# Kernel optimization log

Hardware: AMD Instinct MI355X
Metric: run time of the kernel (lower is better)

Reference implementation:

```python
import jax, jax.numpy as jnp
import numpy as np

N, H, M, B = 64, 64, 32, 16384
relu = jax.nn.relu


def setup_inputs() -> dict:
    key = jax.random.key(0)
    ks = jax.random.split(key, 10)
    s = 0.05
    x = jax.random.normal(ks[0], (B, N), dtype=jnp.float32)
    # stacked per-node weights (torch Linear applies x @ W.T, W: [out, in])
    W1a = jax.random.normal(ks[1], (N, H, N), dtype=jnp.float32) * s   # directed net layer 1
    W1b = jax.random.normal(ks[2], (N, M, H), dtype=jnp.float32) * s   # directed net layer 2
    W2a = jax.random.normal(ks[3], (N, H, N), dtype=jnp.float32) * s   # bi-directed net layer 1
    W2b = jax.random.normal(ks[4], (N, M, H), dtype=jnp.float32) * s   # bi-directed net layer 2
    W3a = jax.random.normal(ks[5], (N, H, 2 * M + N), dtype=jnp.float32) * s  # fuse layer 1
    b3a = jax.random.normal(ks[6], (N, H), dtype=jnp.float32) * s
    W3b = jax.random.normal(ks[7], (N, 1, H), dtype=jnp.float32) * s          # fuse layer 2
    b3b = jax.random.normal(ks[8], (N, 1), dtype=jnp.float32) * s
    return {"x": x, "W1a": W1a, "W1b": W1b, "W2a": W2a, "W2b": W2b,
            "W3a": W3a, "b3a": b3a, "W3b": W3b, "b3b": b3b}


def reference(x, W1a, W1b, W2a, W2b, W3a, b3a, W3b, b3b):
    Bsz, n = x.shape
    eye = jnp.eye(n, dtype=x.dtype)
    off = 1.0 - eye  # filter_1; adjacency at init is also (ones - eye), so mask is idempotent
    # inputs_1_dag / inputs_1_bi: [B, N, N] per-node masked copies of x
    x1 = jnp.einsum('bn,in->bin', x, off)
    # inputs_2: [B, N, N] with x[b,i] on the diagonal of row i
    x2 = eye[None, :, :] * x[:, None, :]
    # directed branch: ReLU(Linear) -> ReLU(Linear), batched over node i
    r1 = relu(jnp.einsum('bih,imh->bim', relu(jnp.einsum('bin,ihn->bih', x1, W1a)), W1b))
    # bi-directed branch (same masked input at init)
    r2 = relu(jnp.einsum('bih,imh->bim', relu(jnp.einsum('bin,ihn->bih', x1, W2a)), W2b))
    feat = jnp.concatenate([r1, r2, x2], axis=2)  # [B, N, 2M+N]
    h = relu(jnp.einsum('bik,ihk->bih', feat, W3a) + b3a[None])
    out = relu(jnp.einsum('bih,ioh->bio', h, W3b) + b3b[None])  # [B, N, 1]
    return out[..., 0]  # [B, N] causal derivative
```

## Files before the change

kernel.cpp:

```cpp
#include <hip/hip_runtime.h>


typedef short bf16x8 __attribute__((ext_vector_type(8)));
typedef float f32x4  __attribute__((ext_vector_type(4)));
typedef unsigned int u32x4 __attribute__((ext_vector_type(4)));

__device__ __forceinline__ unsigned int pack2(float a, float b) {
    union { float f; unsigned int u; } ua, ub; ua.f = a; ub.f = b;
    return __builtin_amdgcn_perm(ub.u + 0x8000u, ua.u + 0x8000u, 0x07060302u);
}

__device__ __forceinline__ f32x4 mfma16(bf16x8 a, bf16x8 b, f32x4 c) {
    return __builtin_amdgcn_mfma_f32_16x16x32_bf16(a, b, c, 0, 0, 0);
}

__device__ __forceinline__ bf16x8 pack_frag(f32x4 lo, f32x4 hi) {
    union { u32x4 u; bf16x8 v; } r;
    r.u[0] = pack2(fmaxf(lo[0], 0.f), fmaxf(lo[1], 0.f));
    r.u[1] = pack2(fmaxf(lo[2], 0.f), fmaxf(lo[3], 0.f));
    r.u[2] = pack2(fmaxf(hi[0], 0.f), fmaxf(hi[1], 0.f));
    r.u[3] = pack2(fmaxf(hi[2], 0.f), fmaxf(hi[3], 0.f));
    return r.v;
}

__device__ __forceinline__ bf16x8 cvt_frag2(const float* __restrict__ plo,
                                            const float* __restrict__ phi) {
    f32x4 f0 = *(const f32x4*)plo;
    f32x4 f1 = *(const f32x4*)phi;
    union { u32x4 u; bf16x8 v; } r;
    r.u[0] = pack2(f0[0], f0[1]);
    r.u[1] = pack2(f0[2], f0[3]);
    r.u[2] = pack2(f1[0], f1[1]);
    r.u[3] = pack2(f1[2], f1[3]);
    return r.v;
}

__device__ __forceinline__ bf16x8 cvt_frag2_m(const float* __restrict__ plo,
                                              const float* __restrict__ phi,
                                              const unsigned int* M) {
    f32x4 f0 = *(const f32x4*)plo;
    f32x4 f1 = *(const f32x4*)phi;
    union { u32x4 u; bf16x8 v; } r;
    r.u[0] = pack2(f0[0], f0[1]) & M[0];
    r.u[1] = pack2(f0[2], f0[3]) & M[1];
    r.u[2] = pack2(f1[0], f1[1]) & M[2];
    r.u[3] = pack2(f1[2], f1[3]) & M[3];
    return r.v;
}

__global__ __launch_bounds__(256) void prep_x(const float* __restrict__ x,
                                              unsigned short* __restrict__ xb) {
    int j = (blockIdx.x * 256 + threadIdx.x) * 8;
    f32x4 a = *(const f32x4*)&x[j];
    f32x4 b = *(const f32x4*)&x[j + 4];
    u32x4 r = { pack2(a[0], a[1]), pack2(a[2], a[3]), pack2(b[0], b[1]), pack2(b[2], b[3]) };
    *(u32x4*)&xb[j] = r;
}

__global__ __launch_bounds__(256, 2) void main_kernel(
    const float* __restrict__ x,
    const float* __restrict__ W1a, const float* __restrict__ W1b,
    const float* __restrict__ W2a, const float* __restrict__ W2b,
    const float* __restrict__ W3a, const float* __restrict__ b3a,
    const float* __restrict__ W3b, const float* __restrict__ b3b,
    const unsigned short* __restrict__ xb,
    float* __restrict__ out)
{
    const int i    = blockIdx.x & 63;
    const int bg   = blockIdx.x >> 6;
    const int tid  = threadIdx.x;
    const int w    = tid >> 6;
    const int lane = tid & 63;
    const int q    = lane >> 4;
    const int c0   = lane & 15;

    unsigned int M[2][4];
    {
        const unsigned int halfmask = (i & 1) ? 0x0000FFFFu : 0xFFFF0000u;
        const int dz = (i >> 1) & 3;
        #pragma unroll
        for (int s = 0; s < 2; ++s) {
            bool hit = ((i >> 3) == s * 4 + q);
            #pragma unroll
            for (int d = 0; d < 4; ++d)
                M[s][d] = (hit && d == dz) ? halfmask : 0xFFFFFFFFu;
        }
    }

    bf16x8 A1[4][2], A2[4][2];
    {
        const float* p1 = W1a + (i << 12);
        const float* p2 = W2a + (i << 12);
        #pragma unroll
        for (int t = 0; t < 4; ++t)
            #pragma unroll
            for (int s = 0; s < 2; ++s) {
                int off = (((t << 4) + c0) << 6) + (s << 5) + (q << 3);
                A1[t][s] = cvt_frag2_m(p1 + off, p1 + off + 4, M[s]);
                A2[t][s] = cvt_frag2_m(p2 + off, p2 + off + 4, M[s]);
            }
    }
    bf16x8 F1[2][2], F2[2][2];
    {
        const float* p1 = W1b + (i << 11);
        const float* p2 = W2b + (i << 11);
        #pragma unroll
        for (int t = 0; t < 2; ++t)
            #pragma unroll
            for (int s = 0; s < 2; ++s) {
                int base = (((t << 4) + c0) << 6) + (s << 5) + (q << 2);
                F1[t][s] = cvt_frag2(p1 + base, p1 + base + 16);
                F2[t][s] = cvt_frag2(p2 + base, p2 + base + 16);
            }
    }
    bf16x8 A3[4][2];
    {
        const float* p3 = W3a + (i << 13);
        #pragma unroll
        for (int t = 0; t < 4; ++t)
            #pragma unroll
            for (int s = 0; s < 2; ++s) {
                int base = (((t << 4) + c0) << 7) + (s << 5) + (q << 2);
                A3[t][s] = cvt_frag2(p3 + base, p3 + base + 16);
            }
    }
    f32x4 b3av[4], w3xv[4], w3bv[4];
    #pragma unroll
    for (int t = 0; t < 4; ++t) {
        int h0 = (i << 6) + (t << 4) + (q << 2);
        b3av[t] = *(const f32x4*)&b3a[h0];
        w3bv[t] = *(const f32x4*)&W3b[h0];
        #pragma unroll
        for (int r = 0; r < 4; ++r)
            w3xv[t][r] = W3a[(i << 13) + (((t << 4) + (q << 2) + r) << 7) + 64 + i];
    }
    const float bb = b3b[i];

    const int rbase0 = (((bg << 2) + w) << 9);

    int row = rbase0 + c0;
    bf16x8 XB0 = *(const bf16x8*)&xb[(row << 6) + (q << 3)];
    bf16x8 XB1 = *(const bf16x8*)&xb[(row << 6) + 32 + (q << 3)];
    float   xd = x[(row << 6) + i];

    for (int k = 0; k < 32; ++k) {
        int nrow = rbase0 + ((k < 31 ? k + 1 : 31) << 4) + c0;
        bf16x8 nXB0 = *(const bf16x8*)&xb[(nrow << 6) + (q << 3)];
        bf16x8 nXB1 = *(const bf16x8*)&xb[(nrow << 6) + 32 + (q << 3)];
        float   nxd = x[(nrow << 6) + i];

        f32x4 a1[4], a2[4];
        #pragma unroll
        for (int t = 0; t < 4; ++t) {
            f32x4 z = {0.f, 0.f, 0.f, 0.f};
            f32x4 u = mfma16(A1[t][0], XB0, z);
            a1[t]   = mfma16(A1[t][1], XB1, u);
            f32x4 v = mfma16(A2[t][0], XB0, z);
            a2[t]   = mfma16(A2[t][1], XB1, v);
        }
        bf16x8 HB0 = pack_frag(a1[0], a1[1]);
        bf16x8 HB1 = pack_frag(a1[2], a1[3]);
        bf16x8 GB0 = pack_frag(a2[0], a2[1]);
        bf16x8 GB1 = pack_frag(a2[2], a2[3]);

        f32x4 b1[2], b2[2];
        #pragma unroll
        for (int t = 0; t < 2; ++t) {
            f32x4 z = {0.f, 0.f, 0.f, 0.f};
            f32x4 u = mfma16(F1[t][0], HB0, z);
            b1[t]   = mfma16(F1[t][1], HB1, u);
            f32x4 v = mfma16(F2[t][0], GB0, z);
            b2[t]   = mfma16(F2[t][1], GB1, v);
        }
        bf16x8 RB0 = pack_frag(b1[0], b1[1]);
        bf16x8 RB1 = pack_frag(b2[0], b2[1]);

        float p = 0.f;
        #pragma unroll
        for (int t = 0; t < 4; ++t) {
            f32x4 acc;
            #pragma unroll
            for (int r = 0; r < 4; ++r) acc[r] = fmaf(xd, w3xv[t][r], b3av[t][r]);
            acc = mfma16(A3[t][0], RB0, acc);
            acc = mfma16(A3[t][1], RB1, acc);
            #pragma unroll
            for (int r = 0; r < 4; ++r) p = fmaf(fmaxf(acc[r], 0.f), w3bv[t][r], p);
        }
        p += __shfl_xor(p, 16);
        p += __shfl_xor(p, 32);
        if (lane < 16) out[(row << 6) + i] = fmaxf(p + bb, 0.f);

        row = nrow; XB0 = nXB0; XB1 = nXB1; xd = nxd;
    }
}

extern "C" void kernel_launch(void* const* d_in, const int* in_sizes, int n_in,
                              void* d_out, int out_size, void* d_ws, size_t ws_size,
                              hipStream_t stream) {
    (void)in_sizes; (void)n_in; (void)out_size; (void)ws_size;
    const float* x   = (const float*)d_in[0];
    const float* W1a = (const float*)d_in[1];
    const float* W1b = (const float*)d_in[2];
    const float* W2a = (const float*)d_in[3];
    const float* W2b = (const float*)d_in[4];
    const float* W3a = (const float*)d_in[5];
    const float* b3a = (const float*)d_in[6];
    const float* W3b = (const float*)d_in[7];
    const float* b3b = (const float*)d_in[8];
    float* out = (float*)d_out;
    unsigned short* xb = (unsigned short*)d_ws;

    prep_x<<<512, 256, 0, stream>>>(x, xb);
    main_kernel<<<512, 256, 0, stream>>>(x, W1a, W1b, W2a, W2b, W3a, b3a, W3b, b3b, xb, out);
}
```

Before: 131.7 us.

## Specialize waves into a three-stage LDS pipeline and fuse x conversion

Splits the per-block work so two waves compute the first layers of each branch, one wave computes the second layers, and one wave computes the fuse layer. Intermediate activations pass through double-buffered shared memory with a block barrier each step. This cuts the per-wave weight register footprint and removes the separate bf16 conversion kernel for x, which is now converted in-register. In exchange it adds a barrier per step, pipeline fill and drain steps, and stores the fuse x-weights in bf16.

New measurement: 171.6 us. 1.3x slower.

```diff
diff --git a/kernel.cpp b/kernel.cpp
--- a/kernel.cpp
+++ b/kernel.cpp
@@ -5,9 +5,18 @@
 typedef float f32x4  __attribute__((ext_vector_type(4)));
 typedef unsigned int u32x4 __attribute__((ext_vector_type(4)));
 
+#define CHUNKS 64
+
 __device__ __forceinline__ unsigned int pack2(float a, float b) {
     union { float f; unsigned int u; } ua, ub; ua.f = a; ub.f = b;
     return __builtin_amdgcn_perm(ub.u + 0x8000u, ua.u + 0x8000u, 0x07060302u);
+}
+
+__device__ __forceinline__ float bf_lo(unsigned int u) {
+    union { unsigned int u; float f; } v; v.u = u << 16; return v.f;
+}
+__device__ __forceinline__ float bf_hi(unsigned int u) {
+    union { unsigned int u; float f; } v; v.u = u & 0xFFFF0000u; return v.f;
 }
 
 __device__ __forceinline__ f32x4 mfma16(bf16x8 a, bf16x8 b, f32x4 c) {
@@ -23,16 +32,18 @@
     return r.v;
 }
 
+__device__ __forceinline__ bf16x8 pack_vals(f32x4 lo, f32x4 hi) {
+    union { u32x4 u; bf16x8 v; } r;
+    r.u[0] = pack2(lo[0], lo[1]);
+    r.u[1] = pack2(lo[2], lo[3]);
+    r.u[2] = pack2(hi[0], hi[1]);
+    r.u[3] = pack2(hi[2], hi[3]);
+    return r.v;
+}
+
 __device__ __forceinline__ bf16x8 cvt_frag2(const float* __restrict__ plo,
                                             const float* __restrict__ phi) {
-    f32x4 f0 = *(const f32x4*)plo;
-    f32x4 f1 = *(const f32x4*)phi;
-    union { u32x4 u; bf16x8 v; } r;
-    r.u[0] = pack2(f0[0], f0[1]);
-    r.u[1] = pack2(f0[2], f0[3]);
-    r.u[2] = pack2(f1[0], f1[1]);
-    r.u[3] = pack2(f1[2], f1[3]);
-    return r.v;
+    return pack_vals(*(const f32x4*)plo, *(const f32x4*)phi);
 }
 
 __device__ __forceinline__ bf16x8 cvt_frag2_m(const float* __restrict__ plo,
@@ -48,31 +59,23 @@
     return r.v;
 }
 
-__global__ __launch_bounds__(256) void prep_x(const float* __restrict__ x,
-                                              unsigned short* __restrict__ xb) {
-    int j = (blockIdx.x * 256 + threadIdx.x) * 8;
-    f32x4 a = *(const f32x4*)&x[j];
-    f32x4 b = *(const f32x4*)&x[j + 4];
-    u32x4 r = { pack2(a[0], a[1]), pack2(a[2], a[3]), pack2(b[0], b[1]), pack2(b[2], b[3]) };
-    *(u32x4*)&xb[j] = r;
-}
-
 __global__ __launch_bounds__(256, 2) void main_kernel(
     const float* __restrict__ x,
     const float* __restrict__ W1a, const float* __restrict__ W1b,
     const float* __restrict__ W2a, const float* __restrict__ W2b,
     const float* __restrict__ W3a, const float* __restrict__ b3a,
     const float* __restrict__ W3b, const float* __restrict__ b3b,
-    const unsigned short* __restrict__ xb,
     float* __restrict__ out)
 {
+    __shared__ unsigned short lds[6144];
+
     const int i    = blockIdx.x & 63;
     const int bg   = blockIdx.x >> 6;
-    const int tid  = threadIdx.x;
-    const int w    = tid >> 6;
-    const int lane = tid & 63;
+    const int w    = threadIdx.x >> 6;
+    const int lane = threadIdx.x & 63;
     const int q    = lane >> 4;
     const int c0   = lane & 15;
+    const int rowbase = bg << 10;
 
     unsigned int M[2][4];
     {
@@ -87,21 +90,17 @@
         }
     }
 
-    bf16x8 A1[4][2], A2[4][2];
-    {
-        const float* p1 = W1a + (i << 12);
-        const float* p2 = W2a + (i << 12);
+    bf16x8 W[8];
+    if (w < 2) {
+        const float* p = (w == 0 ? W1a : W2a) + (i << 12);
         #pragma unroll
         for (int t = 0; t < 4; ++t)
             #pragma unroll
             for (int s = 0; s < 2; ++s) {
                 int off = (((t << 4) + c0) << 6) + (s << 5) + (q << 3);
-                A1[t][s] = cvt_frag2_m(p1 + off, p1 + off + 4, M[s]);
-                A2[t][s] = cvt_frag2_m(p2 + off, p2 + off + 4, M[s]);
-            }
-    }
-    bf16x8 F1[2][2], F2[2][2];
-    {
+                W[t * 2 + s] = cvt_frag2_m(p + off, p + off + 4, M[s]);
+            }
+    } else if (w == 2) {
         const float* p1 = W1b + (i << 11);
         const float* p2 = W2b + (i << 11);
         #pragma unroll
@@ -109,95 +108,128 @@
             #pragma unroll
             for (int s = 0; s < 2; ++s) {
                 int base = (((t << 4) + c0) << 6) + (s << 5) + (q << 2);
-                F1[t][s] = cvt_frag2(p1 + base, p1 + base + 16);
-                F2[t][s] = cvt_frag2(p2 + base, p2 + base + 16);
-            }
-    }
-    bf16x8 A3[4][2];
-    {
+                W[t * 2 + s]     = cvt_frag2(p1 + base, p1 + base + 16);
+                W[4 + t * 2 + s] = cvt_frag2(p2 + base, p2 + base + 16);
+            }
+    } else {
         const float* p3 = W3a + (i << 13);
         #pragma unroll
         for (int t = 0; t < 4; ++t)
             #pragma unroll
             for (int s = 0; s < 2; ++s) {
                 int base = (((t << 4) + c0) << 7) + (s << 5) + (q << 2);
-                A3[t][s] = cvt_frag2(p3 + base, p3 + base + 16);
-            }
-    }
-    f32x4 b3av[4], w3xv[4], w3bv[4];
-    #pragma unroll
-    for (int t = 0; t < 4; ++t) {
-        int h0 = (i << 6) + (t << 4) + (q << 2);
-        b3av[t] = *(const f32x4*)&b3a[h0];
-        w3bv[t] = *(const f32x4*)&W3b[h0];
-        #pragma unroll
-        for (int r = 0; r < 4; ++r)
-            w3xv[t][r] = W3a[(i << 13) + (((t << 4) + (q << 2) + r) << 7) + 64 + i];
-    }
-    const float bb = b3b[i];
-
-    const int rbase0 = (((bg << 2) + w) << 9);
-
-    int row = rbase0 + c0;
-    bf16x8 XB0 = *(const bf16x8*)&xb[(row << 6) + (q << 3)];
-    bf16x8 XB1 = *(const bf16x8*)&xb[(row << 6) + 32 + (q << 3)];
-    float   xd = x[(row << 6) + i];
-
-    for (int k = 0; k < 32; ++k) {
-        int nrow = rbase0 + ((k < 31 ? k + 1 : 31) << 4) + c0;
-        bf16x8 nXB0 = *(const bf16x8*)&xb[(nrow << 6) + (q << 3)];
-        bf16x8 nXB1 = *(const bf16x8*)&xb[(nrow << 6) + 32 + (q << 3)];
-        float   nxd = x[(nrow << 6) + i];
-
-        f32x4 a1[4], a2[4];
+                W[t * 2 + s] = cvt_frag2(p3 + base, p3 + base + 16);
+            }
+    }
+
+    f32x4 b3av[4], w3bv[4];
+    uint2 wxp[4];
+    float bb = 0.f, xd_n = 0.f;
+    if (w == 3) {
         #pragma unroll
         for (int t = 0; t < 4; ++t) {
-            f32x4 z = {0.f, 0.f, 0.f, 0.f};
-            f32x4 u = mfma16(A1[t][0], XB0, z);
-            a1[t]   = mfma16(A1[t][1], XB1, u);
-            f32x4 v = mfma16(A2[t][0], XB0, z);
-            a2[t]   = mfma16(A2[t][1], XB1, v);
+            int h0 = (i << 6) + (t << 4) + (q << 2);
+            b3av[t] = *(const f32x4*)&b3a[h0];
+            w3bv[t] = *(const f32x4*)&W3b[h0];
+            float v0 = W3a[(i << 13) + (((t << 4) + (q << 2) + 0) << 7) + 64 + i];
+            float v1 = W3a[(i << 13) + (((t << 4) + (q << 2) + 1) << 7) + 64 + i];
+            float v2 = W3a[(i << 13) + (((t << 4) + (q << 2) + 2) << 7) + 64 + i];
+            float v3 = W3a[(i << 13) + (((t << 4) + (q << 2) + 3) << 7) + 64 + i];
+            wxp[t].x = pack2(v0, v1);
+            wxp[t].y = pack2(v2, v3);
         }
-        bf16x8 HB0 = pack_frag(a1[0], a1[1]);
-        bf16x8 HB1 = pack_frag(a1[2], a1[3]);
-        bf16x8 GB0 = pack_frag(a2[0], a2[1]);
-        bf16x8 GB1 = pack_frag(a2[2], a2[3]);
-
-        f32x4 b1[2], b2[2];
-        #pragma unroll
-        for (int t = 0; t < 2; ++t) {
-            f32x4 z = {0.f, 0.f, 0.f, 0.f};
-            f32x4 u = mfma16(F1[t][0], HB0, z);
-            b1[t]   = mfma16(F1[t][1], HB1, u);
-            f32x4 v = mfma16(F2[t][0], GB0, z);
-            b2[t]   = mfma16(F2[t][1], GB1, v);
+        bb = b3b[i];
+        xd_n = x[((rowbase + c0) << 6) + i];
+    }
+
+    f32x4 xr0, xr1, xr2, xr3;
+    if (w < 2) {
+        const float* xp = x + ((rowbase + c0) << 6) + (q << 3);
+        xr0 = *(const f32x4*)xp;       xr1 = *(const f32x4*)(xp + 4);
+        xr2 = *(const f32x4*)(xp + 32); xr3 = *(const f32x4*)(xp + 36);
+    }
+
+    for (int k = 0; k < CHUNKS + 2; ++k) {
+        if (w < 2) {
+            if (k < CHUNKS) {
+                bf16x8 XB0 = pack_vals(xr0, xr1);
+                bf16x8 XB1 = pack_vals(xr2, xr3);
+                if (k + 1 < CHUNKS) {
+                    const float* xp = x + ((rowbase + ((k + 1) << 4) + c0) << 6) + (q << 3);
+                    xr0 = *(const f32x4*)xp;        xr1 = *(const f32x4*)(xp + 4);
+                    xr2 = *(const f32x4*)(xp + 32); xr3 = *(const f32x4*)(xp + 36);
+                }
+                f32x4 a[4];
+                #pragma unroll
+                for (int t = 0; t < 4; ++t) {
+                    f32x4 z = {0.f, 0.f, 0.f, 0.f};
+                    f32x4 u = mfma16(W[2 * t], XB0, z);
+                    a[t] = mfma16(W[2 * t + 1], XB1, u);
+                }
+                bf16x8 H0 = pack_frag(a[0], a[1]);
+                bf16x8 H1 = pack_frag(a[2], a[3]);
+                unsigned short* dst = &lds[(w << 11) + ((k & 1) << 10) + (lane << 3)];
+                *(bf16x8*)dst         = H0;
+                *(bf16x8*)(dst + 512) = H1;
+            }
+        } else if (w == 2) {
+            int k2 = k - 1;
+            if (k2 >= 0 && k2 < CHUNKS) {
+                const unsigned short* s1 = &lds[((k2 & 1) << 10) + (lane << 3)];
+                const unsigned short* s2 = s1 + 2048;
+                bf16x8 HB0 = *(const bf16x8*)s1, HB1 = *(const bf16x8*)(s1 + 512);
+                bf16x8 GB0 = *(const bf16x8*)s2, GB1 = *(const bf16x8*)(s2 + 512);
+                f32x4 b1[2], b2[2];
+                #pragma unroll
+                for (int t = 0; t < 2; ++t) {
+                    f32x4 z = {0.f, 0.f, 0.f, 0.f};
+                    f32x4 u = mfma16(W[2 * t], HB0, z);
+                    b1[t] = mfma16(W[2 * t + 1], HB1, u);
+                    f32x4 v = mfma16(W[4 + 2 * t], GB0, z);
+                    b2[t] = mfma16(W[5 + 2 * t], GB1, v);
+                }
+                bf16x8 R0 = pack_frag(b1[0], b1[1]);
+                bf16x8 R1 = pack_frag(b2[0], b2[1]);
+                unsigned short* dst = &lds[4096 + ((k2 & 1) << 10) + (lane << 3)];
+                *(bf16x8*)dst         = R0;
+                *(bf16x8*)(dst + 512) = R1;
+            }
+        } else {
+            int k3 = k - 2;
+            if (k3 >= 0) {
+                float xdc = xd_n;
+                if (k3 + 1 < CHUNKS)
+                    xd_n = x[((rowbase + ((k3 + 1) << 4) + c0) << 6) + i];
+                const unsigned short* s = &lds[4096 + ((k3 & 1) << 10) + (lane << 3)];
+                bf16x8 RB0 = *(const bf16x8*)s, RB1 = *(const bf16x8*)(s + 512);
+                float p = 0.f;
+                #pragma unroll
+                for (int t = 0; t < 4; ++t) {
+                    f32x4 acc;
+                    acc[0] = fmaf(xdc, bf_lo(wxp[t].x), b3av[t][0]);
+                    acc[1] = fmaf(xdc, bf_hi(wxp[t].x), b3av[t][1]);
+                    acc[2] = fmaf(xdc, bf_lo(wxp[t].y), b3av[t][2]);
+                    acc[3] = fmaf(xdc, bf_hi(wxp[t].y), b3av[t][3]);
+                    acc = mfma16(W[2 * t], RB0, acc);
+                    acc = mfma16(W[2 * t + 1], RB1, acc);
+                    #pragma unroll
+                    for (int r = 0; r < 4; ++r)
+                        p = fmaf(fmaxf(acc[r], 0.f), w3bv[t][r], p);
+                }
+                p += __shfl_xor(p, 16);
+                p += __shfl_xor(p, 32);
+                if (lane < 16)
+                    out[((rowbase + (k3 << 4) + c0) << 6) + i] = fmaxf(p + bb, 0.f);
+            }
         }
-        bf16x8 RB0 = pack_frag(b1[0], b1[1]);
-        bf16x8 RB1 = pack_frag(b2[0], b2[1]);
-
-        float p = 0.f;
-        #pragma unroll
-        for (int t = 0; t < 4; ++t) {
-            f32x4 acc;
-            #pragma unroll
-            for (int r = 0; r < 4; ++r) acc[r] = fmaf(xd, w3xv[t][r], b3av[t][r]);
-            acc = mfma16(A3[t][0], RB0, acc);
-            acc = mfma16(A3[t][1], RB1, acc);
-            #pragma unroll
-            for (int r = 0; r < 4; ++r) p = fmaf(fmaxf(acc[r], 0.f), w3bv[t][r], p);
-        }
-        p += __shfl_xor(p, 16);
-        p += __shfl_xor(p, 32);
-        if (lane < 16) out[(row << 6) + i] = fmaxf(p + bb, 0.f);
-
-        row = nrow; XB0 = nXB0; XB1 = nXB1; xd = nxd;
+        __syncthreads();
     }
 }
 
 extern "C" void kernel_launch(void* const* d_in, const int* in_sizes, int n_in,
                               void* d_out, int out_size, void* d_ws, size_t ws_size,
                               hipStream_t stream) {
-    (void)in_sizes; (void)n_in; (void)out_size; (void)ws_size;
+    (void)in_sizes; (void)n_in; (void)out_size; (void)d_ws; (void)ws_size;
     const float* x   = (const float*)d_in[0];
     const float* W1a = (const float*)d_in[1];
     const float* W1b = (const float*)d_in[2];
@@ -208,8 +240,6 @@
     const float* W3b = (const float*)d_in[7];
     const float* b3b = (const float*)d_in[8];
     float* out = (float*)d_out;
-    unsigned short* xb = (unsigned short*)d_ws;
-
-    prep_x<<<512, 256, 0, stream>>>(x, xb);
-    main_kernel<<<512, 256, 0, stream>>>(x, W1a, W1b, W2a, W2b, W3a, b3a, W3b, b3b, xb, out);
-}
+
+    main_kernel<<<1024, 256, 0, stream>>>(x, W1a, W1b, W2a, W2b, W3a, b3a, W3b, b3b, out);
+}
```

## Replace final layer reduction with MFMA and interleave two row streams

Applied to the files above, without the earlier changes.

The final fuse-layer dot product with W3b, previously a per-lane FMA loop followed by two cross-lane shuffles, now runs as two MFMAs against a bf16 fragment of W3b. The W3a diagonal column is packed into bf16 pairs to save registers. The explicit software prefetch of the next row is removed and replaced by two independent row-tile computations per iteration, so the scheduler can overlap loads and MFMA chains. This lowers the final-layer precision to bf16 and relies on the compiler to hide load latency.

Result: slower. 138.0 us (+4.8%).

```diff
diff --git a/kernel.cpp b/kernel.cpp
--- a/kernel.cpp
+++ b/kernel.cpp
@@ -8,6 +8,13 @@
 __device__ __forceinline__ unsigned int pack2(float a, float b) {
     union { float f; unsigned int u; } ua, ub; ua.f = a; ub.f = b;
     return __builtin_amdgcn_perm(ub.u + 0x8000u, ua.u + 0x8000u, 0x07060302u);
+}
+
+__device__ __forceinline__ float bf_lo(unsigned int u) {
+    union { unsigned int u; float f; } v; v.u = u << 16; return v.f;
+}
+__device__ __forceinline__ float bf_hi(unsigned int u) {
+    union { unsigned int u; float f; } v; v.u = u & 0xFFFF0000u; return v.f;
 }
 
 __device__ __forceinline__ f32x4 mfma16(bf16x8 a, bf16x8 b, f32x4 c) {
@@ -124,39 +131,44 @@
                 A3[t][s] = cvt_frag2(p3 + base, p3 + base + 16);
             }
     }
-    f32x4 b3av[4], w3xv[4], w3bv[4];
+    bf16x8 WB[2];
+    {
+        const float* pb = W3b + (i << 6);
+        #pragma unroll
+        for (int s = 0; s < 2; ++s) {
+            int base = (s << 5) + (q << 2);
+            WB[s] = cvt_frag2(pb + base, pb + base + 16);
+        }
+    }
+    f32x4 b3av[4];
+    uint2  wxp[4];
     #pragma unroll
     for (int t = 0; t < 4; ++t) {
         int h0 = (i << 6) + (t << 4) + (q << 2);
         b3av[t] = *(const f32x4*)&b3a[h0];
-        w3bv[t] = *(const f32x4*)&W3b[h0];
-        #pragma unroll
-        for (int r = 0; r < 4; ++r)
-            w3xv[t][r] = W3a[(i << 13) + (((t << 4) + (q << 2) + r) << 7) + 64 + i];
+        float v0 = W3a[(i << 13) + (((t << 4) + (q << 2) + 0) << 7) + 64 + i];
+        float v1 = W3a[(i << 13) + (((t << 4) + (q << 2) + 1) << 7) + 64 + i];
+        float v2 = W3a[(i << 13) + (((t << 4) + (q << 2) + 2) << 7) + 64 + i];
+        float v3 = W3a[(i << 13) + (((t << 4) + (q << 2) + 3) << 7) + 64 + i];
+        wxp[t].x = pack2(v0, v1);
+        wxp[t].y = pack2(v2, v3);
     }
     const float bb = b3b[i];
 
-    const int rbase0 = (((bg << 2) + w) << 9);
-
-    int row = rbase0 + c0;
-    bf16x8 XB0 = *(const bf16x8*)&xb[(row << 6) + (q << 3)];
-    bf16x8 XB1 = *(const bf16x8*)&xb[(row << 6) + 32 + (q << 3)];
-    float   xd = x[(row << 6) + i];
-
-    for (int k = 0; k < 32; ++k) {
-        int nrow = rbase0 + ((k < 31 ? k + 1 : 31) << 4) + c0;
-        bf16x8 nXB0 = *(const bf16x8*)&xb[(nrow << 6) + (q << 3)];
-        bf16x8 nXB1 = *(const bf16x8*)&xb[(nrow << 6) + 32 + (q << 3)];
-        float   nxd = x[(nrow << 6) + i];
+    auto process = [&](int row) {
+        const unsigned short* xp = xb + (row << 6);
+        bf16x8 X0 = *(const bf16x8*)&xp[(q << 3)];
+        bf16x8 X1 = *(const bf16x8*)&xp[32 + (q << 3)];
+        float  xd = x[(row << 6) + i];
 
         f32x4 a1[4], a2[4];
         #pragma unroll
         for (int t = 0; t < 4; ++t) {
             f32x4 z = {0.f, 0.f, 0.f, 0.f};
-            f32x4 u = mfma16(A1[t][0], XB0, z);
-            a1[t]   = mfma16(A1[t][1], XB1, u);
-            f32x4 v = mfma16(A2[t][0], XB0, z);
-            a2[t]   = mfma16(A2[t][1], XB1, v);
+            f32x4 u = mfma16(A1[t][0], X0, z);
+            a1[t]   = mfma16(A1[t][1], X1, u);
+            f32x4 v = mfma16(A2[t][0], X0, z);
+            a2[t]   = mfma16(A2[t][1], X1, v);
         }
         bf16x8 HB0 = pack_frag(a1[0], a1[1]);
         bf16x8 HB1 = pack_frag(a1[2], a1[3]);
@@ -175,22 +187,30 @@
         bf16x8 RB0 = pack_frag(b1[0], b1[1]);
         bf16x8 RB1 = pack_frag(b2[0], b2[1]);
 
-        float p = 0.f;
+        f32x4 acc[4];
         #pragma unroll
         for (int t = 0; t < 4; ++t) {
-            f32x4 acc;
-            #pragma unroll
-            for (int r = 0; r < 4; ++r) acc[r] = fmaf(xd, w3xv[t][r], b3av[t][r]);
-            acc = mfma16(A3[t][0], RB0, acc);
-            acc = mfma16(A3[t][1], RB1, acc);
-            #pragma unroll
-            for (int r = 0; r < 4; ++r) p = fmaf(fmaxf(acc[r], 0.f), w3bv[t][r], p);
-        }
-        p += __shfl_xor(p, 16);
-        p += __shfl_xor(p, 32);
-        if (lane < 16) out[(row << 6) + i] = fmaxf(p + bb, 0.f);
-
-        row = nrow; XB0 = nXB0; XB1 = nXB1; xd = nxd;
+            f32x4 c;
+            c[0] = fmaf(xd, bf_lo(wxp[t].x), b3av[t][0]);
+            c[1] = fmaf(xd, bf_hi(wxp[t].x), b3av[t][1]);
+            c[2] = fmaf(xd, bf_lo(wxp[t].y), b3av[t][2]);
+            c[3] = fmaf(xd, bf_hi(wxp[t].y), b3av[t][3]);
+            c = mfma16(A3[t][0], RB0, c);
+            acc[t] = mfma16(A3[t][1], RB1, c);
+        }
+        bf16x8 HD0 = pack_frag(acc[0], acc[1]);
+        bf16x8 HD1 = pack_frag(acc[2], acc[3]);
+        f32x4 pz = {0.f, 0.f, 0.f, 0.f};
+        pz = mfma16(WB[0], HD0, pz);
+        pz = mfma16(WB[1], HD1, pz);
+        if (lane < 16) out[(row << 6) + i] = fmaxf(pz[0] + bb, 0.f);
+    };
+
+    const int r0 = (((bg << 2) + w) << 9) + c0;
+    for (int k = 0; k < 16; ++k) {
+        int rA = r0 + (k << 4);
+        process(rA);
+        process(rA + 256);
     }
 }
 
```
